# Optimization experiments

Hardware: AMD Instinct MI355X
Metric: run time of the kernel (lower is better)

The kernel has to match this reference:

```python
import jax, jax.numpy as jnp
import numpy as np
from jax import lax

DIM = 128
N_CODEBOOKS = 8
CODEBOOK_SIZE = 2048
BATCH = 16
TOKENS = 2048


def setup_inputs() -> dict:
    key = jax.random.key(0)
    k1, k2 = jax.random.split(key)
    x = jax.random.normal(k1, (BATCH, DIM, TOKENS), dtype=jnp.float32)
    # matches nn.Parameter(torch.randn(K, D) / D**0.5) per stage, stacked
    codebooks = jax.random.normal(k2, (N_CODEBOOKS, CODEBOOK_SIZE, DIM),
                                  dtype=jnp.float32) / jnp.sqrt(jnp.float32(DIM))
    return {"x": x, "codebooks": codebooks}


def reference(x, codebooks):
    """Residual VQ forward.

    x: (B, D, T), codebooks: (n_cb, K, D)
    Returns (total_quantized (B,D,T), codes (B,n_cb,T) int32, commitment_loss scalar)
    """
    xt = jnp.transpose(x, (0, 2, 1))  # (B, T, D)

    def step(carry, cb):
        residual, total = carry  # (B,T,D) each; cb: (K,D)
        # squared euclidean distances: ||r||^2 - 2 r.c + ||c||^2 -> (B,T,K)
        dist = (jnp.sum(residual * residual, axis=-1, keepdims=True)
                - 2.0 * jnp.einsum('btd,kd->btk', residual, cb)
                + jnp.sum(cb * cb, axis=-1))
        idx = jnp.argmin(dist, axis=-1)          # (B, T)
        quantized = cb[idx]                       # gather -> (B, T, D)
        # straight-through combine
        q_st = residual + lax.stop_gradient(quantized - residual)
        total = total + q_st
        residual = residual - lax.stop_gradient(quantized)
        # F.mse_loss(residual.detach(), zeros) == mean(residual**2), detached
        loss = jnp.mean(lax.stop_gradient(residual) ** 2)
        return (residual, total), (idx.astype(jnp.int32), loss)

    init = (xt, jnp.zeros_like(xt))
    (_, total), (codes, losses) = lax.scan(step, init, codebooks)
    total_quantized = jnp.transpose(total, (0, 2, 1))   # (B, D, T)
    codes = jnp.transpose(codes, (1, 0, 2))             # (B, n_cb, T)
    commitment_loss = jnp.sum(losses)
    return total_quantized, codes, commitment_loss
```

## Files before the change

kernel.cpp:

```cpp
#include <hip/hip_runtime.h>

#define DIM 128
#define NCB 8
#define KSZ 2048
#define BATCH 16
#define TOK 2048
#define NTOK (BATCH * TOK)
#define NELEM (BATCH * DIM * TOK)
#define T_TILE 64
#define NTHR 512
#define CHUNK 32
#define HCHUNKS 32

typedef float f32x4 __attribute__((ext_vector_type(4)));
typedef short s16x8 __attribute__((ext_vector_type(8)));

__device__ __forceinline__ unsigned short f2bf(float f) {
    unsigned u = __float_as_uint(f);
    u = (u + 0x7FFFu + ((u >> 16) & 1u)) >> 16;
    return (unsigned short)u;
}
__device__ __forceinline__ float bf2f(unsigned short h) {
    return __uint_as_float(((unsigned)h) << 16);
}

__global__ void rvq_prep_hi(const float* __restrict__ cbs,
                            unsigned short* __restrict__ ch) {
    int i = blockIdx.x * 256 + threadIdx.x;
    ch[i] = f2bf(cbs[i]);
}

__global__ void rvq_cnorm(const float* __restrict__ cbs,
                          float* __restrict__ cnorm,
                          float* __restrict__ loss_acc) {
    if (blockIdx.x == 0 && threadIdx.x == 0) *loss_acc = 0.0f;
    int k = blockIdx.x * 256 + threadIdx.x;
    const float4* row = (const float4*)(cbs + (size_t)k * DIM);
    float s = 0.0f;
#pragma unroll
    for (int i = 0; i < DIM / 4; ++i) {
        float4 v = row[i];
        s += v.x * v.x + v.y * v.y + v.z * v.z + v.w * v.w;
    }
    cnorm[k] = s;
}

__global__ __launch_bounds__(NTHR, 4) void rvq_fused(
        const float* __restrict__ x,
        const float* __restrict__ cbs,
        const unsigned short* __restrict__ ch,
        const float* __restrict__ cng,
        float* __restrict__ out,
        float* __restrict__ codes,
        float* __restrict__ loss_acc) {
    __shared__ float res_lds[T_TILE][DIM + 2];
    __shared__ unsigned short Bbuf[2][4096];
    __shared__ float mv1[T_TILE * 32];
    __shared__ float mv2[T_TILE * 32];
    __shared__ unsigned short mi1[T_TILE * 32];
    __shared__ unsigned short mi2[T_TILE * 32];
    __shared__ unsigned short best4s[T_TILE][4];

    const int tid   = threadIdx.x;
    const int lane  = tid & 63;
    const int wv    = __builtin_amdgcn_readfirstlane(tid >> 6);
    const int col16 = lane & 15;
    const int quad  = lane >> 4;
    const int h2    = wv & 1;
    const int wg    = wv >> 1;

    const int token0 = blockIdx.x * T_TILE;
    const int b      = token0 >> 11;
    const int t_in_b = token0 & (TOK - 1);

    {
        const float* xb = x + (size_t)b * DIM * TOK + t_in_b;
#pragma unroll
        for (int it = 0; it < 4; ++it) {
            int idx = it * NTHR + tid;
            int d  = idx >> 4;
            int t4 = (idx & 15) * 4;
            float4 v = *(const float4*)(xb + (size_t)d * TOK + t4);
            res_lds[t4 + 0][d] = v.x;
            res_lds[t4 + 1][d] = v.y;
            res_lds[t4 + 2][d] = v.z;
            res_lds[t4 + 3][d] = v.w;
        }
    }
    __syncthreads();

    float my_loss = 0.0f;

#define STAGE_LOAD(cc)                                                         \
    {                                                                          \
        const int _f0 = wg * 2, _f1 = wg * 2 + 1;                              \
        stg0 = *(const s16x8*)(ch_s +                                          \
            ((size_t)(h2 * 1024 + (cc) * CHUNK + (_f0 >> 2) * 16 + col16)) * DIM + \
            ((_f0 & 3) * 32 + quad * 8));                                      \
        stg1 = *(const s16x8*)(ch_s +                                          \
            ((size_t)(h2 * 1024 + (cc) * CHUNK + (_f1 >> 2) * 16 + col16)) * DIM + \
            ((_f1 & 3) * 32 + quad * 8));                                      \
    }

#define STAGE_WRITE()                                                          \
    {                                                                          \
        *(s16x8*)&Bbuf[h2][(wg * 2 + 0) * 512 + lane * 8] = stg0;              \
        *(s16x8*)&Bbuf[h2][(wg * 2 + 1) * 512 + lane * 8] = stg1;              \
    }

#define COMPUTE_FOLD(cc)                                                       \
    {                                                                          \
        f32x4 a0 = (f32x4){0.f, 0.f, 0.f, 0.f};                                \
        f32x4 a1 = a0;                                                         \
        _Pragma("unroll")                                                      \
        for (int dc = 0; dc < 4; ++dc) {                                       \
            s16x8 b0 = *(const s16x8*)&Bbuf[h2][(0 + dc) * 512 + lane * 8];    \
            s16x8 b1 = *(const s16x8*)&Bbuf[h2][(4 + dc) * 512 + lane * 8];    \
            a0 = __builtin_amdgcn_mfma_f32_16x16x32_bf16(ah[dc], b0, a0, 0, 0, 0); \
            a0 = __builtin_amdgcn_mfma_f32_16x16x32_bf16(al[dc], b0, a0, 0, 0, 0); \
            a1 = __builtin_amdgcn_mfma_f32_16x16x32_bf16(ah[dc], b1, a1, 0, 0, 0); \
            a1 = __builtin_amdgcn_mfma_f32_16x16x32_bf16(al[dc], b1, a1, 0, 0, 0); \
        }                                                                      \
        const int _ib0 = h2 * 1024 + (cc) * CHUNK + col16;                     \
        const float _cn0 = cn_s[_ib0], _cn1 = cn_s[_ib0 + 16];                 \
        _Pragma("unroll")                                                      \
        for (int r = 0; r < 4; ++r) {                                          \
            float p0 = fmaf(-2.0f, a0[r], _cn0);                               \
            float p1 = fmaf(-2.0f, a1[r], _cn1);                               \
            bool q1 = p0 < v1[r];                                              \
            bool q2 = p0 < v2[r];                                              \
            v2[r] = q1 ? v1[r] : (q2 ? p0 : v2[r]);                            \
            i2[r] = q1 ? i1[r] : (q2 ? _ib0 : i2[r]);                          \
            v1[r] = q1 ? p0 : v1[r];                                           \
            i1[r] = q1 ? _ib0 : i1[r];                                         \
            bool w1 = p1 < v1[r];                                              \
            bool w2 = p1 < v2[r];                                              \
            v2[r] = w1 ? v1[r] : (w2 ? p1 : v2[r]);                            \
            i2[r] = w1 ? i1[r] : (w2 ? (_ib0 + 16) : i2[r]);                   \
            v1[r] = w1 ? p1 : v1[r];                                           \
            i1[r] = w1 ? (_ib0 + 16) : i1[r];                                  \
        }                                                                      \
    }

#pragma unroll 1
    for (int s = 0; s < NCB; ++s) {
        const unsigned short* __restrict__ ch_s = ch  + (size_t)s * KSZ * DIM;
        const float* __restrict__ cb_s = cbs + (size_t)s * KSZ * DIM;
        const float* __restrict__ cn_s = cng + (size_t)s * KSZ;

        s16x8 stg0, stg1;

        STAGE_LOAD(0);

        s16x8 ah[4], al[4];
#pragma unroll
        for (int dc = 0; dc < 4; ++dc) {
            int t  = wg * 16 + col16;
            int d0 = dc * 32 + quad * 8;
            float4 u = *(const float4*)&res_lds[t][d0];
            float4 w = *(const float4*)&res_lds[t][d0 + 4];
            float e[8] = {u.x, u.y, u.z, u.w, w.x, w.y, w.z, w.w};
            s16x8 hv, lv;
#pragma unroll
            for (int j = 0; j < 8; ++j) {
                unsigned short hb = f2bf(e[j]);
                hv[j] = (short)hb;
                lv[j] = (short)f2bf(e[j] - bf2f(hb));
            }
            ah[dc] = hv; al[dc] = lv;
        }

        float v1[4], v2[4]; int i1[4], i2[4];
#pragma unroll
        for (int r = 0; r < 4; ++r) {
            v1[r] = 3.4e38f; v2[r] = 3.4e38f; i1[r] = 0; i2[r] = 0;
        }

        STAGE_WRITE(); __syncthreads();
#pragma unroll 1
        for (int cc = 0; cc < HCHUNKS - 1; ++cc) {
            STAGE_LOAD(cc + 1);
            COMPUTE_FOLD(cc);
            __syncthreads();
            STAGE_WRITE();
            __syncthreads();
        }
        COMPUTE_FOLD(HCHUNKS - 1);

#pragma unroll
        for (int r = 0; r < 4; ++r) {
            int t = wg * 16 + quad * 4 + r;
            int o = t * 32 + h2 * 16 + col16;
            mv1[o] = v1[r];
            mi1[o] = (unsigned short)i1[r];
            mv2[o] = v2[r];
            mi2[o] = (unsigned short)i2[r];
        }
        __syncthreads();

        {
            const int mt = tid >> 3;
            const int c8 = tid & 7;
            float bv[4] = {3.4e38f, 3.4e38f, 3.4e38f, 3.4e38f};
            int   bi[4] = {0x7FFFFFFF, 0x7FFFFFFF, 0x7FFFFFFF, 0x7FFFFFFF};
            const float* MV = (c8 & 4) ? mv2 : mv1;
            const unsigned short* MI = (c8 & 4) ? mi2 : mi1;
            const int base = mt * 32 + (c8 & 3) * 8;
            const float4 va = *(const float4*)&MV[base];
            const float4 vb = *(const float4*)&MV[base + 4];
            const s16x8  qi = *(const s16x8*)&MI[base];
            float vv[8] = {va.x, va.y, va.z, va.w, vb.x, vb.y, vb.z, vb.w};
#pragma unroll
            for (int c = 0; c < 8; ++c) {
                float v = vv[c]; int i = (int)(unsigned short)qi[c];
#pragma unroll
                for (int j = 0; j < 4; ++j) {
                    if (v < bv[j] || (v == bv[j] && i < bi[j])) {
                        float tv = bv[j]; bv[j] = v; v = tv;
                        int   ti = bi[j]; bi[j] = i; i = ti;
                    }
                }
            }
#pragma unroll
            for (int mk = 1; mk <= 4; mk <<= 1) {
                float ov[4]; int oi[4];
#pragma unroll
                for (int j = 0; j < 4; ++j) {
                    ov[j] = __shfl_xor(bv[j], mk, 64);
                    oi[j] = __shfl_xor(bi[j], mk, 64);
                }
#pragma unroll
                for (int c = 0; c < 4; ++c) {
                    float v = ov[c]; int i = oi[c];
#pragma unroll
                    for (int j = 0; j < 4; ++j) {
                        if (v < bv[j] || (v == bv[j] && i < bi[j])) {
                            float tv = bv[j]; bv[j] = v; v = tv;
                            int   ti = bi[j]; bi[j] = i; i = ti;
                        }
                    }
                }
            }
            if (c8 < 4) best4s[mt][c8] = (unsigned short)bi[c8];
        }
        __syncthreads();

        {
            const int t  = tid >> 3;
            const int c8 = tid & 7;
            const int cand = best4s[t][c8 & 3];
            const float* crow = cb_s + (size_t)cand * DIM;
            float n0 = 0, n1 = 0, n2 = 0, n3 = 0;
            float a0 = 0, a1 = 0, a2 = 0, a3 = 0;
#pragma unroll 8
            for (int d4 = 0; d4 < DIM / 4; ++d4) {
                float4 r4 = *(const float4*)&res_lds[t][d4 * 4];
                float4 q4 = *(const float4*)&crow[d4 * 4];
                n0 = fmaf(r4.x, r4.x, n0); n1 = fmaf(r4.y, r4.y, n1);
                n2 = fmaf(r4.z, r4.z, n2); n3 = fmaf(r4.w, r4.w, n3);
                a0 = fmaf(r4.x, q4.x, a0); a1 = fmaf(r4.y, q4.y, a1);
                a2 = fmaf(r4.z, q4.z, a2); a3 = fmaf(r4.w, q4.w, a3);
            }
            float rn  = (n0 + n1) + (n2 + n3);
            float dot = (a0 + a1) + (a2 + a3);
            float dist = fmaf(-2.0f, dot, rn) + cn_s[cand];
            int best = cand;
#pragma unroll
            for (int mk = 1; mk <= 2; mk <<= 1) {
                float od = __shfl_xor(dist, mk, 64);
                int   oi = __shfl_xor(best, mk, 64);
                if (od < dist || (od == dist && oi < best)) {
                    dist = od; best = oi;
                }
            }
            if (c8 == 0)
                codes[(size_t)b * (NCB * TOK) + (size_t)s * TOK + t_in_b + t] =
                    (float)best;
            const float* qrow = cb_s + (size_t)best * DIM;
            float lp = 0.0f;
#pragma unroll
            for (int k4 = 0; k4 < 4; ++k4) {
                int d = c8 * 16 + k4 * 4;
                float4 r4 = *(const float4*)&res_lds[t][d];
                float4 q4 = *(const float4*)&qrow[d];
                float4 nr;
                nr.x = r4.x - q4.x; nr.y = r4.y - q4.y;
                nr.z = r4.z - q4.z; nr.w = r4.w - q4.w;
                *(float4*)&res_lds[t][d] = nr;
                lp += nr.x * nr.x + nr.y * nr.y + nr.z * nr.z + nr.w * nr.w;
            }
            my_loss += lp;
        }
        __syncthreads();
    }

    {
        const float* xb = x + (size_t)b * DIM * TOK + t_in_b;
        float* ob = out + (size_t)b * DIM * TOK + t_in_b;
#pragma unroll
        for (int it = 0; it < 4; ++it) {
            int idx = it * NTHR + tid;
            int d  = idx >> 4;
            int t4 = (idx & 15) * 4;
            float4 v = *(const float4*)(xb + (size_t)d * TOK + t4);
            float4 o;
            o.x = v.x - res_lds[t4 + 0][d];
            o.y = v.y - res_lds[t4 + 1][d];
            o.z = v.z - res_lds[t4 + 2][d];
            o.w = v.w - res_lds[t4 + 3][d];
            *(float4*)(ob + (size_t)d * TOK + t4) = o;
        }
    }

#pragma unroll
    for (int off = 32; off > 0; off >>= 1)
        my_loss += __shfl_down(my_loss, off, 64);
    if (lane == 0) atomicAdd(loss_acc, my_loss);
}

__global__ void rvq_loss_fin(const float* __restrict__ loss_acc,
                             float* __restrict__ loss_out) {
    *loss_out = *loss_acc * (1.0f / (float)NELEM);
}

extern "C" void kernel_launch(void* const* d_in, const int* in_sizes, int n_in,
                              void* d_out, int out_size, void* d_ws, size_t ws_size,
                              hipStream_t stream) {
    const float* x   = (const float*)d_in[0];
    const float* cbs = (const float*)d_in[1];

    float* out      = (float*)d_out;
    float* codes    = out + NELEM;
    float* loss_out = out + NELEM + (size_t)BATCH * NCB * TOK;

    float* wsf      = (float*)d_ws;
    float* loss_acc = wsf;
    unsigned short* ch = (unsigned short*)(wsf + 256);
    float* cng = (float*)(ch + (size_t)NCB * KSZ * DIM);

    hipLaunchKernelGGL(rvq_prep_hi, dim3((NCB * KSZ * DIM) / 256), dim3(256),
                       0, stream, cbs, ch);
    hipLaunchKernelGGL(rvq_cnorm, dim3((NCB * KSZ) / 256), dim3(256), 0, stream,
                       cbs, cng, loss_acc);
    hipLaunchKernelGGL(rvq_fused, dim3(NTOK / T_TILE), dim3(NTHR), 0, stream,
                       x, cbs, ch, cng, out, codes, loss_acc);
    hipLaunchKernelGGL(rvq_loss_fin, dim3(1), dim3(1), 0, stream,
                       loss_acc, loss_out);
}
```

Measured before the change: 571.8 us.

## Double codebook chunk size per pipeline step and pre-reduce candidates before top-2 fold

Doubles the codebook chunk staged per iteration from 32 to 64 entries, so each half of the codebook is processed in 16 steps instead of 32, halving the number of barrier pairs. Each wave now issues four independent MFMA accumulator chains per chunk. The four candidates are first reduced to a single min before updating the running top-2, which cuts the select work per candidate. To fit the larger staging buffer, the LDS arrays for the B buffer and the reduction scratch are aliased into one union, which needs an extra barrier. The risks are higher register pressure, possible occupancy loss under launch_bounds(512,4), and a changed second-best candidate set: when two candidates in the same group of four both beat the running best, only the smaller one is kept.

Result: no change. 574.4 us (+0.5%).

```diff
diff --git a/kernel.cpp b/kernel.cpp
--- a/kernel.cpp
+++ b/kernel.cpp
@@ -9,8 +9,8 @@
 #define NELEM (BATCH * DIM * TOK)
 #define T_TILE 64
 #define NTHR 512
-#define CHUNK 32
-#define HCHUNKS 32
+#define CHUNK 64
+#define HCHUNKS 16
 
 typedef float f32x4 __attribute__((ext_vector_type(4)));
 typedef short s16x8 __attribute__((ext_vector_type(8)));
@@ -54,12 +54,13 @@
         float* __restrict__ codes,
         float* __restrict__ loss_acc) {
     __shared__ float res_lds[T_TILE][DIM + 2];
-    __shared__ unsigned short Bbuf[2][4096];
-    __shared__ float mv1[T_TILE * 32];
-    __shared__ float mv2[T_TILE * 32];
-    __shared__ unsigned short mi1[T_TILE * 32];
-    __shared__ unsigned short mi2[T_TILE * 32];
-    __shared__ unsigned short best4s[T_TILE][4];
+    __shared__ __align__(16) unsigned char uni[32768];
+    unsigned short* Bb = (unsigned short*)uni;
+    float*          mv1 = (float*)uni;
+    float*          mv2 = (float*)(uni + 8192);
+    unsigned short* mi1 = (unsigned short*)(uni + 16384);
+    unsigned short* mi2 = (unsigned short*)(uni + 20480);
+    unsigned short (*best4s)[4] = (unsigned short(*)[4])(uni + 24576);
 
     const int tid   = threadIdx.x;
     const int lane  = tid & 63;
@@ -93,52 +94,65 @@
 
 #define STAGE_LOAD(cc)                                                         \
     {                                                                          \
-        const int _f0 = wg * 2, _f1 = wg * 2 + 1;                              \
-        stg0 = *(const s16x8*)(ch_s +                                          \
-            ((size_t)(h2 * 1024 + (cc) * CHUNK + (_f0 >> 2) * 16 + col16)) * DIM + \
-            ((_f0 & 3) * 32 + quad * 8));                                      \
-        stg1 = *(const s16x8*)(ch_s +                                          \
-            ((size_t)(h2 * 1024 + (cc) * CHUNK + (_f1 >> 2) * 16 + col16)) * DIM + \
-            ((_f1 & 3) * 32 + quad * 8));                                      \
+        const unsigned short* _p = ch_s +                                      \
+            ((size_t)(h2 * 1024 + (cc) * CHUNK + wg * 16 + col16)) * DIM +     \
+            quad * 8;                                                          \
+        stg0 = *(const s16x8*)(_p + 0);                                        \
+        stg1 = *(const s16x8*)(_p + 32);                                       \
+        stg2 = *(const s16x8*)(_p + 64);                                       \
+        stg3 = *(const s16x8*)(_p + 96);                                       \
     }
 
 #define STAGE_WRITE()                                                          \
     {                                                                          \
-        *(s16x8*)&Bbuf[h2][(wg * 2 + 0) * 512 + lane * 8] = stg0;              \
-        *(s16x8*)&Bbuf[h2][(wg * 2 + 1) * 512 + lane * 8] = stg1;              \
+        unsigned short* _bh = Bb + h2 * 8192;                                  \
+        *(s16x8*)&_bh[(wg * 4 + 0) * 512 + lane * 8] = stg0;                   \
+        *(s16x8*)&_bh[(wg * 4 + 1) * 512 + lane * 8] = stg1;                   \
+        *(s16x8*)&_bh[(wg * 4 + 2) * 512 + lane * 8] = stg2;                   \
+        *(s16x8*)&_bh[(wg * 4 + 3) * 512 + lane * 8] = stg3;                   \
     }
 
 #define COMPUTE_FOLD(cc)                                                       \
     {                                                                          \
+        const unsigned short* _bh = Bb + h2 * 8192;                            \
         f32x4 a0 = (f32x4){0.f, 0.f, 0.f, 0.f};                                \
-        f32x4 a1 = a0;                                                         \
+        f32x4 a1 = a0, a2 = a0, a3 = a0;                                       \
         _Pragma("unroll")                                                      \
         for (int dc = 0; dc < 4; ++dc) {                                       \
-            s16x8 b0 = *(const s16x8*)&Bbuf[h2][(0 + dc) * 512 + lane * 8];    \
-            s16x8 b1 = *(const s16x8*)&Bbuf[h2][(4 + dc) * 512 + lane * 8];    \
+            s16x8 b0 = *(const s16x8*)&_bh[(0  + dc) * 512 + lane * 8];        \
+            s16x8 b1 = *(const s16x8*)&_bh[(4  + dc) * 512 + lane * 8];        \
+            s16x8 b2 = *(const s16x8*)&_bh[(8  + dc) * 512 + lane * 8];        \
+            s16x8 b3 = *(const s16x8*)&_bh[(12 + dc) * 512 + lane * 8];        \
             a0 = __builtin_amdgcn_mfma_f32_16x16x32_bf16(ah[dc], b0, a0, 0, 0, 0); \
+            a1 = __builtin_amdgcn_mfma_f32_16x16x32_bf16(ah[dc], b1, a1, 0, 0, 0); \
+            a2 = __builtin_amdgcn_mfma_f32_16x16x32_bf16(ah[dc], b2, a2, 0, 0, 0); \
+            a3 = __builtin_amdgcn_mfma_f32_16x16x32_bf16(ah[dc], b3, a3, 0, 0, 0); \
             a0 = __builtin_amdgcn_mfma_f32_16x16x32_bf16(al[dc], b0, a0, 0, 0, 0); \
-            a1 = __builtin_amdgcn_mfma_f32_16x16x32_bf16(ah[dc], b1, a1, 0, 0, 0); \
             a1 = __builtin_amdgcn_mfma_f32_16x16x32_bf16(al[dc], b1, a1, 0, 0, 0); \
+            a2 = __builtin_amdgcn_mfma_f32_16x16x32_bf16(al[dc], b2, a2, 0, 0, 0); \
+            a3 = __builtin_amdgcn_mfma_f32_16x16x32_bf16(al[dc], b3, a3, 0, 0, 0); \
         }                                                                      \
         const int _ib0 = h2 * 1024 + (cc) * CHUNK + col16;                     \
         const float _cn0 = cn_s[_ib0], _cn1 = cn_s[_ib0 + 16];                 \
+        const float _cn2 = cn_s[_ib0 + 32], _cn3 = cn_s[_ib0 + 48];            \
         _Pragma("unroll")                                                      \
         for (int r = 0; r < 4; ++r) {                                          \
             float p0 = fmaf(-2.0f, a0[r], _cn0);                               \
             float p1 = fmaf(-2.0f, a1[r], _cn1);                               \
-            bool q1 = p0 < v1[r];                                              \
-            bool q2 = p0 < v2[r];                                              \
-            v2[r] = q1 ? v1[r] : (q2 ? p0 : v2[r]);                            \
-            i2[r] = q1 ? i1[r] : (q2 ? _ib0 : i2[r]);                          \
-            v1[r] = q1 ? p0 : v1[r];                                           \
-            i1[r] = q1 ? _ib0 : i1[r];                                         \
-            bool w1 = p1 < v1[r];                                              \
-            bool w2 = p1 < v2[r];                                              \
-            v2[r] = w1 ? v1[r] : (w2 ? p1 : v2[r]);                            \
-            i2[r] = w1 ? i1[r] : (w2 ? (_ib0 + 16) : i2[r]);                   \
-            v1[r] = w1 ? p1 : v1[r];                                           \
-            i1[r] = w1 ? (_ib0 + 16) : i1[r];                                  \
+            float p2 = fmaf(-2.0f, a2[r], _cn2);                               \
+            float p3 = fmaf(-2.0f, a3[r], _cn3);                               \
+            bool c01 = p1 < p0;                                                \
+            float m01 = c01 ? p1 : p0; int j01 = c01 ? _ib0 + 16 : _ib0;       \
+            bool c23 = p3 < p2;                                                \
+            float m23 = c23 ? p3 : p2; int j23 = c23 ? _ib0 + 48 : _ib0 + 32;  \
+            bool cf = m23 < m01;                                               \
+            float m = cf ? m23 : m01; int jm = cf ? j23 : j01;                 \
+            bool b1 = m < v1[r];                                               \
+            bool b2 = m < v2[r];                                               \
+            v2[r] = b1 ? v1[r] : (b2 ? m : v2[r]);                             \
+            i2[r] = b1 ? i1[r] : (b2 ? jm : i2[r]);                            \
+            v1[r] = b1 ? m : v1[r];                                            \
+            i1[r] = b1 ? jm : i1[r];                                           \
         }                                                                      \
     }
 
@@ -148,7 +162,7 @@
         const float* __restrict__ cb_s = cbs + (size_t)s * KSZ * DIM;
         const float* __restrict__ cn_s = cng + (size_t)s * KSZ;
 
-        s16x8 stg0, stg1;
+        s16x8 stg0, stg1, stg2, stg3;
 
         STAGE_LOAD(0);
 
@@ -186,6 +200,7 @@
             __syncthreads();
         }
         COMPUTE_FOLD(HCHUNKS - 1);
+        __syncthreads();
 
 #pragma unroll
         for (int r = 0; r < 4; ++r) {
```

## Load codebook fragments directly to registers, removing LDS staging and barriers

Applied to the files above, without the earlier changes.

Drops the shared-memory double buffer for bf16 codebook tiles. Each wave now loads its MFMA B fragments straight from global memory into registers, with a two-deep register prefetch, which removes two __syncthreads per chunk. The hi and lo MFMA products go into separate accumulators that are summed at the end, giving two independent MFMA chains. The cost is more redundant global/L2 traffic, since the 4 wave groups sharing a half each load the same codebook rows, and higher register pressure.

After: 1.161 ms. +103.1%, slower.

```diff
diff --git a/kernel.cpp b/kernel.cpp
--- a/kernel.cpp
+++ b/kernel.cpp
@@ -9,8 +9,7 @@
 #define NELEM (BATCH * DIM * TOK)
 #define T_TILE 64
 #define NTHR 512
-#define CHUNK 32
-#define HCHUNKS 32
+#define NRG 64
 
 typedef float f32x4 __attribute__((ext_vector_type(4)));
 typedef short s16x8 __attribute__((ext_vector_type(8)));
@@ -54,7 +53,6 @@
         float* __restrict__ codes,
         float* __restrict__ loss_acc) {
     __shared__ float res_lds[T_TILE][DIM + 2];
-    __shared__ unsigned short Bbuf[2][4096];
     __shared__ float mv1[T_TILE * 32];
     __shared__ float mv2[T_TILE * 32];
     __shared__ unsigned short mi1[T_TILE * 32];
@@ -91,54 +89,41 @@
 
     float my_loss = 0.0f;
 
-#define STAGE_LOAD(cc)                                                         \
+#define LOADRG(buf, cnreg, rg)                                                 \
     {                                                                          \
-        const int _f0 = wg * 2, _f1 = wg * 2 + 1;                              \
-        stg0 = *(const s16x8*)(ch_s +                                          \
-            ((size_t)(h2 * 1024 + (cc) * CHUNK + (_f0 >> 2) * 16 + col16)) * DIM + \
-            ((_f0 & 3) * 32 + quad * 8));                                      \
-        stg1 = *(const s16x8*)(ch_s +                                          \
-            ((size_t)(h2 * 1024 + (cc) * CHUNK + (_f1 >> 2) * 16 + col16)) * DIM + \
-            ((_f1 & 3) * 32 + quad * 8));                                      \
-    }
-
-#define STAGE_WRITE()                                                          \
+        const unsigned short* _p = pB + (size_t)(rg) * (16 * DIM);             \
+        buf[0] = *(const s16x8*)(_p + 0);                                      \
+        buf[1] = *(const s16x8*)(_p + 32);                                     \
+        buf[2] = *(const s16x8*)(_p + 64);                                     \
+        buf[3] = *(const s16x8*)(_p + 96);                                     \
+        cnreg = pCN[(rg) * 16];                                                \
+    }
+
+#define COMPUTE_RG(buf, cnreg, rg, REFILL)                                     \
     {                                                                          \
-        *(s16x8*)&Bbuf[h2][(wg * 2 + 0) * 512 + lane * 8] = stg0;              \
-        *(s16x8*)&Bbuf[h2][(wg * 2 + 1) * 512 + lane * 8] = stg1;              \
-    }
-
-#define COMPUTE_FOLD(cc)                                                       \
-    {                                                                          \
-        f32x4 a0 = (f32x4){0.f, 0.f, 0.f, 0.f};                                \
-        f32x4 a1 = a0;                                                         \
-        _Pragma("unroll")                                                      \
-        for (int dc = 0; dc < 4; ++dc) {                                       \
-            s16x8 b0 = *(const s16x8*)&Bbuf[h2][(0 + dc) * 512 + lane * 8];    \
-            s16x8 b1 = *(const s16x8*)&Bbuf[h2][(4 + dc) * 512 + lane * 8];    \
-            a0 = __builtin_amdgcn_mfma_f32_16x16x32_bf16(ah[dc], b0, a0, 0, 0, 0); \
-            a0 = __builtin_amdgcn_mfma_f32_16x16x32_bf16(al[dc], b0, a0, 0, 0, 0); \
-            a1 = __builtin_amdgcn_mfma_f32_16x16x32_bf16(ah[dc], b1, a1, 0, 0, 0); \
-            a1 = __builtin_amdgcn_mfma_f32_16x16x32_bf16(al[dc], b1, a1, 0, 0, 0); \
-        }                                                                      \
-        const int _ib0 = h2 * 1024 + (cc) * CHUNK + col16;                     \
-        const float _cn0 = cn_s[_ib0], _cn1 = cn_s[_ib0 + 16];                 \
+        f32x4 axh = (f32x4){0.f, 0.f, 0.f, 0.f};                               \
+        f32x4 axl = (f32x4){0.f, 0.f, 0.f, 0.f};                               \
+        axh = __builtin_amdgcn_mfma_f32_16x16x32_bf16(ah[0], buf[0], axh, 0, 0, 0); \
+        axl = __builtin_amdgcn_mfma_f32_16x16x32_bf16(al[0], buf[0], axl, 0, 0, 0); \
+        axh = __builtin_amdgcn_mfma_f32_16x16x32_bf16(ah[1], buf[1], axh, 0, 0, 0); \
+        axl = __builtin_amdgcn_mfma_f32_16x16x32_bf16(al[1], buf[1], axl, 0, 0, 0); \
+        axh = __builtin_amdgcn_mfma_f32_16x16x32_bf16(ah[2], buf[2], axh, 0, 0, 0); \
+        axl = __builtin_amdgcn_mfma_f32_16x16x32_bf16(al[2], buf[2], axl, 0, 0, 0); \
+        axh = __builtin_amdgcn_mfma_f32_16x16x32_bf16(ah[3], buf[3], axh, 0, 0, 0); \
+        axl = __builtin_amdgcn_mfma_f32_16x16x32_bf16(al[3], buf[3], axl, 0, 0, 0); \
+        const float _cnu = cnreg;                                              \
+        const int _idx = h2 * 1024 + (rg) * 16 + col16;                        \
+        REFILL;                                                                \
+        f32x4 ax = axh + axl;                                                  \
         _Pragma("unroll")                                                      \
         for (int r = 0; r < 4; ++r) {                                          \
-            float p0 = fmaf(-2.0f, a0[r], _cn0);                               \
-            float p1 = fmaf(-2.0f, a1[r], _cn1);                               \
-            bool q1 = p0 < v1[r];                                              \
-            bool q2 = p0 < v2[r];                                              \
-            v2[r] = q1 ? v1[r] : (q2 ? p0 : v2[r]);                            \
-            i2[r] = q1 ? i1[r] : (q2 ? _ib0 : i2[r]);                          \
-            v1[r] = q1 ? p0 : v1[r];                                           \
-            i1[r] = q1 ? _ib0 : i1[r];                                         \
-            bool w1 = p1 < v1[r];                                              \
-            bool w2 = p1 < v2[r];                                              \
-            v2[r] = w1 ? v1[r] : (w2 ? p1 : v2[r]);                            \
-            i2[r] = w1 ? i1[r] : (w2 ? (_ib0 + 16) : i2[r]);                   \
-            v1[r] = w1 ? p1 : v1[r];                                           \
-            i1[r] = w1 ? (_ib0 + 16) : i1[r];                                  \
+            float p = fmaf(-2.0f, ax[r], _cnu);                                \
+            bool b1 = p < v1[r];                                               \
+            bool b2 = p < v2[r];                                               \
+            v2[r] = b1 ? v1[r] : (b2 ? p : v2[r]);                             \
+            i2[r] = b1 ? i1[r] : (b2 ? _idx : i2[r]);                          \
+            v1[r] = b1 ? p : v1[r];                                            \
+            i1[r] = b1 ? _idx : i1[r];                                         \
         }                                                                      \
     }
 
@@ -148,9 +133,9 @@
         const float* __restrict__ cb_s = cbs + (size_t)s * KSZ * DIM;
         const float* __restrict__ cn_s = cng + (size_t)s * KSZ;
 
-        s16x8 stg0, stg1;
-
-        STAGE_LOAD(0);
+        const unsigned short* pB =
+            ch_s + (size_t)(h2 * 1024 + col16) * DIM + quad * 8;
+        const float* pCN = cn_s + h2 * 1024 + col16;
 
         s16x8 ah[4], al[4];
 #pragma unroll
@@ -176,16 +161,17 @@
             v1[r] = 3.4e38f; v2[r] = 3.4e38f; i1[r] = 0; i2[r] = 0;
         }
 
-        STAGE_WRITE(); __syncthreads();
+        s16x8 bA[4], bB[4];
+        float cnA, cnB;
+        LOADRG(bA, cnA, 0);
+        LOADRG(bB, cnB, 1);
 #pragma unroll 1
-        for (int cc = 0; cc < HCHUNKS - 1; ++cc) {
-            STAGE_LOAD(cc + 1);
-            COMPUTE_FOLD(cc);
-            __syncthreads();
-            STAGE_WRITE();
-            __syncthreads();
-        }
-        COMPUTE_FOLD(HCHUNKS - 1);
+        for (int rg = 0; rg < NRG; rg += 2) {
+            COMPUTE_RG(bA, cnA, rg,
+                       if (rg + 2 < NRG) { LOADRG(bA, cnA, rg + 2); });
+            COMPUTE_RG(bB, cnB, rg + 1,
+                       if (rg + 3 < NRG) { LOADRG(bB, cnB, rg + 3); });
+        }
 
 #pragma unroll
         for (int r = 0; r < 4; ++r) {
```
